# Kernel optimization log

Hardware: AMD Instinct MI355X
Metric: run time of the kernel (lower is better)

The kernel has to match this reference:

```python
import jax, jax.numpy as jnp
import numpy as np

B, S, D = 2, 2048, 1024  # batch, seq, model_dim
E, K, H = 8, 2, 4096     # experts, top_k, expert hidden
CAP_FACTOR = 1.0


def setup_inputs() -> dict:
    key = jax.random.key(0)
    ks = jax.random.split(key, 6)
    scale_in = 1.0 / np.sqrt(D)
    scale_h = 1.0 / np.sqrt(H)
    return {
        "x": jax.random.normal(ks[0], (B, S, D), jnp.float32),
        "wg": jax.random.normal(ks[1], (D, E), jnp.float32) * scale_in,
        "w1": jax.random.normal(ks[2], (E, D, H), jnp.float32) * scale_in,
        "b1": jnp.zeros((E, H), jnp.float32),
        "w2": jax.random.normal(ks[3], (E, H, D), jnp.float32) * scale_h,
        "b2": jnp.zeros((E, D), jnp.float32),
    }


def _moe_forward(x, wg, w1, b1, w2, b2):
    Bb, Ss, Dd = x.shape
    T = Bb * Ss
    cap = int(K * CAP_FACTOR * ((T + E - 1) // E))  # Tutel capacity rule
    xt = x.reshape(T, Dd)

    # ---- gating ----
    logits = xt @ wg                      # [T, E]
    scores = jax.nn.softmax(logits, axis=-1)
    gates_k, idx_k = jax.lax.top_k(scores, K)  # [T, K]
    # normalize_gate=True: renormalize top-k gates
    gates_k = gates_k / jnp.sum(gates_k, axis=-1, keepdims=True)

    # ---- GShard-style location assignment (slot-major cumsum) ----
    masks = jax.nn.one_hot(idx_k, E, dtype=jnp.int32)           # [T, K, E]
    m = jnp.transpose(masks, (1, 0, 2)).reshape(K * T, E)       # slot-major
    locs_full = jnp.cumsum(m, axis=0) - 1                       # [K*T, E]
    loc = jnp.sum(locs_full * m, axis=-1)                       # [K*T]
    loc = loc.reshape(K, T).T                                   # [T, K]
    valid = (loc < cap).astype(xt.dtype)                        # capacity drop
    loc_c = jnp.clip(loc, 0, cap - 1)

    # ---- dispatch: scatter tokens into [E, cap, D] ----
    contrib = (xt[:, None, :] * valid[:, :, None]).reshape(T * K, Dd)
    disp = jnp.zeros((E, cap, Dd), xt.dtype)
    disp = disp.at[idx_k.reshape(-1), loc_c.reshape(-1)].add(contrib)

    # ---- grouped expert FFN ----
    h = jax.nn.relu(jnp.einsum("ecd,edh->ech", disp, w1) + b1[:, None, :])
    out = jnp.einsum("ech,ehd->ecd", h, w2) + b2[:, None, :]

    # ---- combine (postscore): gather + gate-weighted sum ----
    gathered = out[idx_k, loc_c]                                # [T, K, D]
    y = jnp.einsum("tk,tkd->td", gates_k * valid, gathered)
    return y.reshape(Bb, Ss, Dd)


def reference(x, wg, w1, b1, w2, b2):
    return _moe_forward(x, wg, w1, b1, w2, b2)
```

## Files before the change

kernel.cpp:

```cpp
#include <hip/hip_runtime.h>
#include <stdint.h>

#define NTOK 4096
#define DIM  1024
#define NEXP 8
#define HID  4096
#define CAP  1024

typedef __bf16 bf16x8 __attribute__((ext_vector_type(8)));
typedef float  f32x4  __attribute__((ext_vector_type(4)));

__device__ __forceinline__ unsigned short f2bf(float f) {
  unsigned int u = __float_as_uint(f);
  return (unsigned short)((u + 0x7fffu + ((u >> 16) & 1u)) >> 16);
}

__device__ __forceinline__ float bf2f(unsigned int bits16) {
  return __uint_as_float(bits16 << 16);
}

__device__ __forceinline__ void load_lds16(const void* g, void* l) {
  __builtin_amdgcn_global_load_lds(
      (__attribute__((address_space(1))) void*)g,
      (__attribute__((address_space(3))) void*)l,
      16, 0, 0);
}

__global__ void gating_kernel(const float* __restrict__ x, const float* __restrict__ wg,
                              int* __restrict__ tok_e, float* __restrict__ tok_g) {
  const int t = blockIdx.x;
  const int l = threadIdx.x;
  float acc[NEXP];
#pragma unroll
  for (int e = 0; e < NEXP; ++e) acc[e] = 0.f;

  const float4* x4  = (const float4*)(x + (size_t)t * DIM);
  const float4* wg4 = (const float4*)wg;
#pragma unroll
  for (int i = 0; i < 4; ++i) {
    int dq = i * 64 + l;
    float4 xv = x4[dq];
    float xs[4] = {xv.x, xv.y, xv.z, xv.w};
#pragma unroll
    for (int c = 0; c < 4; ++c) {
      int d = dq * 4 + c;
      float4 wa = wg4[d * 2], wb = wg4[d * 2 + 1];
      acc[0] += xs[c] * wa.x; acc[1] += xs[c] * wa.y;
      acc[2] += xs[c] * wa.z; acc[3] += xs[c] * wa.w;
      acc[4] += xs[c] * wb.x; acc[5] += xs[c] * wb.y;
      acc[6] += xs[c] * wb.z; acc[7] += xs[c] * wb.w;
    }
  }
#pragma unroll
  for (int off = 32; off; off >>= 1)
#pragma unroll
    for (int e = 0; e < NEXP; ++e) acc[e] += __shfl_xor(acc[e], off);

  if (l == 0) {
    float m = acc[0];
#pragma unroll
    for (int e = 1; e < NEXP; ++e) m = fmaxf(m, acc[e]);
    float p[NEXP];
#pragma unroll
    for (int e = 0; e < NEXP; ++e) p[e] = __expf(acc[e] - m);
    int e0 = 0; float b0 = p[0];
#pragma unroll
    for (int e = 1; e < NEXP; ++e) if (p[e] > b0) { b0 = p[e]; e0 = e; }
    int e1 = -1; float b1v = -1.f;
#pragma unroll
    for (int e = 0; e < NEXP; ++e) if (e != e0 && p[e] > b1v) { b1v = p[e]; e1 = e; }
    float inv = 1.f / (b0 + b1v);
    tok_e[2 * t] = e0; tok_e[2 * t + 1] = e1;
    tok_g[2 * t] = b0 * inv; tok_g[2 * t + 1] = b1v * inv;
  }
}

__global__ void scan_kernel(const int* __restrict__ tok_e, int* __restrict__ tok_loc,
                            int* __restrict__ slot_map) {
  const int l = threadIdx.x;
  const unsigned long long below = (1ull << l) - 1ull;
  int base[NEXP];
#pragma unroll
  for (int e = 0; e < NEXP; ++e) base[e] = 0;

  int nxt = tok_e[((0 * 64 + l) & (NTOK - 1)) * 2 + ((0 * 64 + l) >> 12)];
  for (int it = 0; it < 128; ++it) {
    int e = nxt;
    if (it + 1 < 128) {
      int g2 = (it + 1) * 64 + l;
      nxt = tok_e[(g2 & (NTOK - 1)) * 2 + (g2 >> 12)];
    }
    int loc = 0;
#pragma unroll
    for (int ex = 0; ex < NEXP; ++ex) {
      unsigned long long msk = __ballot(e == ex);
      int off = __popcll(msk & below);
      if (e == ex) loc = base[ex] + off;
      base[ex] += __popcll(msk);
    }
    int g = it * 64 + l;
    int k = g >> 12, t = g & (NTOK - 1);
    bool valid = loc < CAP;
    tok_loc[t * 2 + k] = valid ? loc : -1;
    if (valid) slot_map[e * CAP + loc] = t;
  }
#pragma unroll
  for (int ex = 0; ex < NEXP; ++ex) {
    int c = base[ex] < CAP ? base[ex] : CAP;
    for (int i = c + l; i < CAP; i += 64) slot_map[ex * CAP + i] = -1;
  }
}

__global__ void dispatch_kernel(const float* __restrict__ x, const int* __restrict__ slot_map,
                                unsigned short* __restrict__ disp) {
  const int s = blockIdx.x;
  const int tid = threadIdx.x;
  int t = slot_map[s];
  uint2 o;
  if (t >= 0) {
    float4 v = ((const float4*)(x + (size_t)t * DIM))[tid];
    o.x = (unsigned)f2bf(v.x) | ((unsigned)f2bf(v.y) << 16);
    o.y = (unsigned)f2bf(v.z) | ((unsigned)f2bf(v.w) << 16);
  } else {
    o.x = 0u; o.y = 0u;
  }
  ((uint2*)(disp + (size_t)s * DIM))[tid] = o;
}

__global__ void transpose_cvt(const float* __restrict__ in, unsigned short* __restrict__ out,
                              int R, int C) {
  __shared__ float tile[64][65];
  const int e = blockIdx.z;
  const float* inp = in + (size_t)e * R * C;
  unsigned short* outp = out + (size_t)e * R * C;
  const int c0 = blockIdx.x * 64, r0 = blockIdx.y * 64;
  const int t = threadIdx.x;
#pragma unroll
  for (int i = 0; i < 4; ++i) {
    int idx = i * 256 + t;
    int r = idx >> 4;
    int c4 = (idx & 15) * 4;
    float4 v = *(const float4*)(inp + (size_t)(r0 + r) * C + c0 + c4);
    tile[r][c4 + 0] = v.x; tile[r][c4 + 1] = v.y;
    tile[r][c4 + 2] = v.z; tile[r][c4 + 3] = v.w;
  }
  __syncthreads();
#pragma unroll
  for (int i = 0; i < 4; ++i) {
    int idx = i * 256 + t;
    int c = idx >> 4;
    int r4 = (idx & 15) * 4;
    float a = tile[r4 + 0][c], b = tile[r4 + 1][c];
    float d0 = tile[r4 + 2][c], d1 = tile[r4 + 3][c];
    uint2 o;
    o.x = (unsigned)f2bf(a) | ((unsigned)f2bf(b) << 16);
    o.y = (unsigned)f2bf(d0) | ((unsigned)f2bf(d1) << 16);
    *(uint2*)(outp + (size_t)(c0 + c) * R + r0 + r4) = o;
  }
}

template <bool RELU, int MB, int NB>
__global__ __launch_bounds__(256)
void gemm_kernel(const unsigned short* __restrict__ A, const unsigned short* __restrict__ B,
                 const float* __restrict__ bias, unsigned short* __restrict__ C,
                 int N, int K) {
  constexpr int M = 1024;
  const int bid = blockIdx.x;
  const int e = bid / (MB * NB);
  const int r = bid - e * (MB * NB);
  const int patch = r / (MB * 4);
  const int q = r - patch * (MB * 4);
  const int mtile = q >> 2;
  const int ntile = patch * 4 + (q & 3);

  A += (size_t)e * M * K;
  B += (size_t)e * N * K;
  bias += (size_t)e * N;
  C += (size_t)e * M * N;
  const int m0 = mtile * 128;
  const int n0 = ntile * 128;
  const int tid = threadIdx.x;
  const int wave = tid >> 6, lane = tid & 63;
  const int wm = wave >> 1, wn = wave & 1;

  __shared__ __align__(16) unsigned short As[2][128 * 64];
  __shared__ __align__(16) unsigned short Bs[2][128 * 64];

  const int srow = lane >> 3;
  const int scol = (lane & 7) * 8;
  const unsigned short* gA = A + (size_t)(m0 + wave * 8 + srow) * K + scol;
  const unsigned short* gB = B + (size_t)(n0 + wave * 8 + srow) * K + scol;
  const int lbase = (wave * 8) * 64;

  f32x4 acc[4][4] = {};

  const int quad = lane >> 4;
  const int arow = (wm * 64 + (lane & 15)) * 64 + quad * 8;
  const int brow = (wn * 64 + (lane & 15)) * 64 + quad * 8;

#pragma unroll
  for (int i = 0; i < 4; ++i) {
    load_lds16(gA + (size_t)i * 32 * K, &As[0][lbase + i * 32 * 64]);
    load_lds16(gB + (size_t)i * 32 * K, &Bs[0][lbase + i * 32 * 64]);
  }
  gA += 64; gB += 64;

  const int nIter = K >> 6;
  for (int it = 0; it < nIter; ++it) {
    const int cur = it & 1;
    __syncthreads();
    if (it + 1 < nIter) {
#pragma unroll
      for (int i = 0; i < 4; ++i) {
        load_lds16(gA + (size_t)i * 32 * K, &As[cur ^ 1][lbase + i * 32 * 64]);
        load_lds16(gB + (size_t)i * 32 * K, &Bs[cur ^ 1][lbase + i * 32 * 64]);
      }
      gA += 64; gB += 64;
    }
#pragma unroll
    for (int kk = 0; kk < 64; kk += 32) {
      bf16x8 af[4], bfr[4];
#pragma unroll
      for (int i = 0; i < 4; ++i)
        af[i] = *reinterpret_cast<const bf16x8*>(&As[cur][arow + i * 16 * 64 + kk]);
#pragma unroll
      for (int j = 0; j < 4; ++j)
        bfr[j] = *reinterpret_cast<const bf16x8*>(&Bs[cur][brow + j * 16 * 64 + kk]);
#pragma unroll
      for (int i = 0; i < 4; ++i)
#pragma unroll
        for (int j = 0; j < 4; ++j)
          acc[i][j] = __builtin_amdgcn_mfma_f32_16x16x32_bf16(af[i], bfr[j], acc[i][j], 0, 0, 0);
    }
  }

  const int crow = m0 + wm * 64 + quad * 4;
  const int ccol = n0 + wn * 64 + (lane & 15);
#pragma unroll
  for (int j = 0; j < 4; ++j) {
    float bj = bias[ccol + j * 16];
#pragma unroll
    for (int i = 0; i < 4; ++i) {
#pragma unroll
      for (int rr = 0; rr < 4; ++rr) {
        float v = acc[i][j][rr] + bj;
        if (RELU) v = fmaxf(v, 0.f);
        C[(size_t)(crow + i * 16 + rr) * N + (ccol + j * 16)] = f2bf(v);
      }
    }
  }
}

__global__ void combine_kernel(const unsigned short* __restrict__ outb,
                               const int* __restrict__ tok_e, const int* __restrict__ tok_loc,
                               const float* __restrict__ tok_g, float* __restrict__ y) {
  const int t = blockIdx.x;
  const int tid = threadIdx.x;
  int e0 = tok_e[2 * t], e1 = tok_e[2 * t + 1];
  int l0 = tok_loc[2 * t], l1 = tok_loc[2 * t + 1];
  float g0 = tok_g[2 * t], g1 = tok_g[2 * t + 1];
  float ax = 0.f, ay = 0.f, az = 0.f, aw = 0.f;
  if (l0 >= 0) {
    uint2 u = ((const uint2*)(outb + ((size_t)e0 * CAP + l0) * DIM))[tid];
    ax += g0 * bf2f(u.x & 0xffffu); ay += g0 * __uint_as_float(u.x & 0xffff0000u);
    az += g0 * bf2f(u.y & 0xffffu); aw += g0 * __uint_as_float(u.y & 0xffff0000u);
  }
  if (l1 >= 0) {
    uint2 u = ((const uint2*)(outb + ((size_t)e1 * CAP + l1) * DIM))[tid];
    ax += g1 * bf2f(u.x & 0xffffu); ay += g1 * __uint_as_float(u.x & 0xffff0000u);
    az += g1 * bf2f(u.y & 0xffffu); aw += g1 * __uint_as_float(u.y & 0xffff0000u);
  }
  float4 o; o.x = ax; o.y = ay; o.z = az; o.w = aw;
  ((float4*)(y + (size_t)t * DIM))[tid] = o;
}

extern "C" void kernel_launch(void* const* d_in, const int* in_sizes, int n_in,
                              void* d_out, int out_size, void* d_ws, size_t ws_size,
                              hipStream_t stream) {
  const float* x  = (const float*)d_in[0];
  const float* wg = (const float*)d_in[1];
  const float* w1 = (const float*)d_in[2];
  const float* b1 = (const float*)d_in[3];
  const float* w2 = (const float*)d_in[4];
  const float* b2 = (const float*)d_in[5];
  float* y = (float*)d_out;

  char* ws = (char*)d_ws;
  int*   tok_e    = (int*)(ws);
  int*   tok_loc  = (int*)(ws + 32768);
  float* tok_g    = (float*)(ws + 65536);
  int*   slot_map = (int*)(ws + 98304);
  unsigned short* disp = (unsigned short*)(ws + 131072);
  unsigned short* wbuf = (unsigned short*)(ws + 131072 + (16ull << 20));
  unsigned short* h    = (unsigned short*)(ws + 131072 + (80ull << 20));
  unsigned short* outb = (unsigned short*)(ws + 131072 + (144ull << 20));

  gating_kernel<<<NTOK, 64, 0, stream>>>(x, wg, tok_e, tok_g);
  scan_kernel<<<1, 64, 0, stream>>>(tok_e, tok_loc, slot_map);
  dispatch_kernel<<<NEXP * CAP, 256, 0, stream>>>(x, slot_map, disp);
  transpose_cvt<<<dim3(HID / 64, DIM / 64, NEXP), 256, 0, stream>>>(w1, wbuf, DIM, HID);
  gemm_kernel<true, 8, 32><<<NEXP * 8 * 32, 256, 0, stream>>>(disp, wbuf, b1, h, HID, DIM);
  transpose_cvt<<<dim3(DIM / 64, HID / 64, NEXP), 256, 0, stream>>>(w2, wbuf, HID, DIM);
  gemm_kernel<false, 8, 8><<<NEXP * 8 * 8, 256, 0, stream>>>(h, wbuf, b2, outb, DIM, HID);
  combine_kernel<<<NTOK, 256, 0, stream>>>(outb, tok_e, tok_loc, tok_g, y);
}
```

Baseline: 580.3 us.

## Swizzle GEMM LDS tiles, stage epilogue through LDS, widen transpose stores

The GEMM now XOR-swizzles the k-column chunk per row, both when loading global data into LDS and when reading fragments for MFMA. The aim is to remove LDS bank conflicts on the 16-byte fragment reads. The epilogue writes the bias/ReLU results into a padded LDS scratch per wave and then emits 16-byte coalesced global stores instead of scattered 2-byte stores. The weight transpose kernel also writes 8 bf16 values per thread with uint4 stores, and the extra syncs plus LDS staging add some latency.

```diff
diff --git a/kernel.cpp b/kernel.cpp
--- a/kernel.cpp
+++ b/kernel.cpp
@@ -138,24 +138,25 @@
 #pragma unroll
   for (int i = 0; i < 4; ++i) {
     int idx = i * 256 + t;
-    int r = idx >> 4;
-    int c4 = (idx & 15) * 4;
+    int r = idx >> 4, c4 = (idx & 15) * 4;
     float4 v = *(const float4*)(inp + (size_t)(r0 + r) * C + c0 + c4);
     tile[r][c4 + 0] = v.x; tile[r][c4 + 1] = v.y;
     tile[r][c4 + 2] = v.z; tile[r][c4 + 3] = v.w;
   }
   __syncthreads();
 #pragma unroll
-  for (int i = 0; i < 4; ++i) {
+  for (int i = 0; i < 2; ++i) {
     int idx = i * 256 + t;
-    int c = idx >> 4;
-    int r4 = (idx & 15) * 4;
-    float a = tile[r4 + 0][c], b = tile[r4 + 1][c];
-    float d0 = tile[r4 + 2][c], d1 = tile[r4 + 3][c];
-    uint2 o;
-    o.x = (unsigned)f2bf(a) | ((unsigned)f2bf(b) << 16);
-    o.y = (unsigned)f2bf(d0) | ((unsigned)f2bf(d1) << 16);
-    *(uint2*)(outp + (size_t)(c0 + c) * R + r0 + r4) = o;
+    int c = idx >> 3, r8 = (idx & 7) * 8;
+    unsigned short s[8];
+#pragma unroll
+    for (int j = 0; j < 8; ++j) s[j] = f2bf(tile[r8 + j][c]);
+    uint4 o;
+    o.x = (unsigned)s[0] | ((unsigned)s[1] << 16);
+    o.y = (unsigned)s[2] | ((unsigned)s[3] << 16);
+    o.z = (unsigned)s[4] | ((unsigned)s[5] << 16);
+    o.w = (unsigned)s[6] | ((unsigned)s[7] << 16);
+    *(uint4*)(outp + (size_t)(c0 + c) * R + r0 + r8) = o;
   }
 }
 
@@ -187,7 +188,7 @@
   __shared__ __align__(16) unsigned short Bs[2][128 * 64];
 
   const int srow = lane >> 3;
-  const int scol = (lane & 7) * 8;
+  const int scol = ((lane & 7) ^ (srow & 7)) * 8;
   const unsigned short* gA = A + (size_t)(m0 + wave * 8 + srow) * K + scol;
   const unsigned short* gB = B + (size_t)(n0 + wave * 8 + srow) * K + scol;
   const int lbase = (wave * 8) * 64;
@@ -195,8 +196,9 @@
   f32x4 acc[4][4] = {};
 
   const int quad = lane >> 4;
-  const int arow = (wm * 64 + (lane & 15)) * 64 + quad * 8;
-  const int brow = (wn * 64 + (lane & 15)) * 64 + quad * 8;
+  const int lxor = lane & 7;
+  const int arowb = (wm * 64 + (lane & 15)) * 64;
+  const int browb = (wn * 64 + (lane & 15)) * 64;
 
 #pragma unroll
   for (int i = 0; i < 4; ++i) {
@@ -219,13 +221,14 @@
     }
 #pragma unroll
     for (int kk = 0; kk < 64; kk += 32) {
+      const int coff = ((quad + (kk >> 3)) ^ lxor) * 8;
       bf16x8 af[4], bfr[4];
 #pragma unroll
       for (int i = 0; i < 4; ++i)
-        af[i] = *reinterpret_cast<const bf16x8*>(&As[cur][arow + i * 16 * 64 + kk]);
+        af[i] = *reinterpret_cast<const bf16x8*>(&As[cur][arowb + i * 16 * 64 + coff]);
 #pragma unroll
       for (int j = 0; j < 4; ++j)
-        bfr[j] = *reinterpret_cast<const bf16x8*>(&Bs[cur][brow + j * 16 * 64 + kk]);
+        bfr[j] = *reinterpret_cast<const bf16x8*>(&Bs[cur][browb + j * 16 * 64 + coff]);
 #pragma unroll
       for (int i = 0; i < 4; ++i)
 #pragma unroll
@@ -234,20 +237,29 @@
     }
   }
 
-  const int crow = m0 + wm * 64 + quad * 4;
-  const int ccol = n0 + wn * 64 + (lane & 15);
+  __syncthreads();
+  unsigned short* scr = (wave < 2 ? &As[0][0] : &Bs[0][0]) + (wave & 1) * 4608;
+  const int lc = lane & 15;
 #pragma unroll
   for (int j = 0; j < 4; ++j) {
-    float bj = bias[ccol + j * 16];
-#pragma unroll
-    for (int i = 0; i < 4; ++i) {
+    float bj = bias[n0 + wn * 64 + j * 16 + lc];
+#pragma unroll
+    for (int i = 0; i < 4; ++i)
 #pragma unroll
       for (int rr = 0; rr < 4; ++rr) {
         float v = acc[i][j][rr] + bj;
         if (RELU) v = fmaxf(v, 0.f);
-        C[(size_t)(crow + i * 16 + rr) * N + (ccol + j * 16)] = f2bf(v);
+        scr[(i * 16 + quad * 4 + rr) * 72 + j * 16 + lc] = f2bf(v);
       }
-    }
+  }
+  __asm__ volatile("s_waitcnt lgkmcnt(0)" ::: "memory");
+  const int erow = lane >> 3;
+  const int ecol = (lane & 7) * 8;
+  unsigned short* Cbase = C + (size_t)(m0 + wm * 64) * N + n0 + wn * 64;
+#pragma unroll
+  for (int p = 0; p < 8; ++p) {
+    uint4 v = *(const uint4*)&scr[(p * 8 + erow) * 72 + ecol];
+    *(uint4*)&Cbase[(size_t)(p * 8 + erow) * N + ecol] = v;
   }
 }
 
```

After: 540.5 us. 1.07x faster.
